# Kernel optimization log

Measured on AMD Instinct MI355X. Metric: run time of the kernel, lower is better.

Reference implementation:

```python
import jax, jax.numpy as jnp
import numpy as np
from jax import lax

DIM, HEADS, BS, TOPK, WIN = 256, 8, 8, 4, 7
HID = 2 * DIM  # DBFFN ffn_expansion_factor=2
B, H, W = 2, 56, 56


def _lin(x, w, b=None):
    # torch Linear: y = x @ W.T + b, W is [out, in]
    y = jnp.einsum('...c,oc->...o', x, w)
    return y if b is None else y + b


def _ln(x, w, b, eps=1e-6):
    mu = jnp.mean(x, -1, keepdims=True)
    var = jnp.mean((x - mu) ** 2, -1, keepdims=True)
    return (x - mu) * lax.rsqrt(var + eps) * w + b


def _mha(Q, K, V, wq_w, wq_b, wk_w, wk_b, wv_w, wv_b, p_w, p_b):
    # standard cross MHA: Q [B,Nq,C], K/V [B,Nk,C]
    Bq, Nq, C = Q.shape
    h, d = HEADS, C // HEADS
    scale = d ** -0.5
    q = _lin(Q, wq_w, wq_b).reshape(Bq, Nq, h, d)
    k = _lin(K, wk_w, wk_b).reshape(Bq, -1, h, d)
    v = _lin(V, wv_w, wv_b).reshape(Bq, -1, h, d)
    attn = jax.nn.softmax(jnp.einsum('bnhd,bmhd->bhnm', q, k) * scale, axis=-1)
    out = jnp.einsum('bhnm,bmhd->bnhd', attn, v).reshape(Bq, Nq, C)
    return _lin(out, p_w, p_b)


def setup_inputs() -> dict:
    key = jax.random.key(0)
    ks = jax.random.split(key, 16)
    s = 0.02
    C = DIM
    inp = {
        'x': jax.random.normal(ks[0], (B, C, H, W), jnp.float32),
        'pos_w': jax.random.normal(ks[1], (C, 1, 3, 3), jnp.float32) * s,
        'pos_b': jnp.zeros((C,), jnp.float32),
        'n1_w': jnp.ones((C,), jnp.float32), 'n1_b': jnp.zeros((C,), jnp.float32),
        'n2_w': jnp.ones((C,), jnp.float32), 'n2_b': jnp.zeros((C,), jnp.float32),
        'wq_w': jax.random.normal(ks[2], (3, C, C), jnp.float32) * s,
        'wq_b': jnp.zeros((3, C), jnp.float32),
        'wk_w': jax.random.normal(ks[3], (3, C, C), jnp.float32) * s,
        'wk_b': jnp.zeros((3, C), jnp.float32),
        'wv_w': jax.random.normal(ks[4], (3, C, C), jnp.float32) * s,
        'wv_b': jnp.zeros((3, C), jnp.float32),
        'pj_w': jax.random.normal(ks[5], (3, C, C), jnp.float32) * s,
        'pj_b': jnp.zeros((3, C), jnp.float32),
        # block scorer
        's1_w': jax.random.normal(ks[6], (C // 2, C), jnp.float32) * s,
        's1_b': jnp.zeros((C // 2,), jnp.float32),
        's2_w': jax.random.normal(ks[7], (1, C // 2), jnp.float32) * s,
        's2_b': jnp.zeros((1,), jnp.float32),
        # gating: per-token softmax weights over 3 branches
        'g_w': jax.random.normal(ks[8], (3, C), jnp.float32) * s,
        'g_b': jnp.zeros((3,), jnp.float32),
        # DBFFN (gated dconv FFN, bias=False): in-proj C->2*HID, dw 3x3, out-proj HID->C
        'pin_w': jax.random.normal(ks[9], (2 * HID, C), jnp.float32) * s,
        'dw_w': jax.random.normal(ks[10], (3, 3, 1, 2 * HID), jnp.float32) * s,
        'pout_w': jax.random.normal(ks[11], (C, HID), jnp.float32) * s,
    }
    return inp


def _forward(x, pos_w, pos_b, n1_w, n1_b, n2_w, n2_b, wq_w, wq_b, wk_w, wk_b,
             wv_w, wv_b, pj_w, pj_b, s1_w, s1_b, s2_w, s2_b, g_w, g_b,
             pin_w, dw_w, pout_w):
    Bx, C, Hx, Wx = x.shape
    # depthwise positional conv
    pos = lax.conv_general_dilated(x, pos_w, (1, 1), 'SAME',
                                   dimension_numbers=('NCHW', 'OIHW', 'NCHW'),
                                   feature_group_count=C)
    x = x + pos + pos_b[None, :, None, None] * 0 + pos_b[None, :, None, None]
    feat = jnp.transpose(x, (0, 2, 3, 1))  # NHWC
    Nq = Hx * Wx
    Q = feat.reshape(Bx, Nq, C)
    # block means
    nH, nW = Hx // BS, Wx // BS
    nB = nH * nW
    blk = feat.reshape(Bx, nH, BS, nW, BS, C).transpose(0, 1, 3, 2, 4, 5)
    blk = blk.reshape(Bx, nB, BS * BS, C).mean(axis=2)  # [B,nB,C]
    # block scores + top-k selection
    hsc = jax.nn.gelu(_lin(blk, s1_w, s1_b), approximate=False)
    scores = _lin(hsc, s2_w, s2_b)[..., 0]  # [B,nB]
    topk = min(TOPK, nB)
    _, idx = lax.top_k(scores, topk)
    K_sel = jnp.take_along_axis(blk, idx[:, :, None], axis=1)  # [B,topk,C]
    # compressed + selected branches
    y_cmp = _mha(Q, blk, blk, wq_w[0], wq_b[0], wk_w[0], wk_b[0], wv_w[0], wv_b[0], pj_w[0], pj_b[0])
    y_sel = _mha(Q, K_sel, K_sel, wq_w[1], wq_b[1], wk_w[1], wk_b[1], wv_w[1], wv_b[1], pj_w[1], pj_b[1])
    # local window branch (replicate-pad + unfold == shifted slices)
    pad = WIN // 2
    padded = jnp.pad(feat, ((0, 0), (pad, pad), (pad, pad), (0, 0)), mode='edge')
    patches = jnp.stack([padded[:, dy:dy + Hx, dx:dx + Wx, :]
                         for dy in range(WIN) for dx in range(WIN)], axis=3)
    patches = patches.reshape(Bx, Nq, WIN * WIN, C)  # [B,Nq,49,C]
    h, d = HEADS, C // HEADS
    scale = d ** -0.5
    q = _lin(Q, wq_w[2], wq_b[2]).reshape(Bx, Nq, h, d)
    k = _lin(patches, wk_w[2], wk_b[2]).reshape(Bx, Nq, WIN * WIN, h, d)
    v = _lin(patches, wv_w[2], wv_b[2]).reshape(Bx, Nq, WIN * WIN, h, d)
    attn = jax.nn.softmax(jnp.einsum('bnhd,bnwhd->bnhw', q, k) * scale, axis=-1)
    y_win = jnp.einsum('bnhw,bnwhd->bnhd', attn, v).reshape(Bx, Nq, C)
    y_win = _lin(y_win, pj_w[2], pj_b[2])
    # gated fusion + residual
    qn = _ln(Q, n1_w, n1_b)
    g = jax.nn.softmax(_lin(qn, g_w, g_b), axis=-1)  # [B,Nq,3]
    y = g[..., 0:1] * y_cmp + g[..., 1:2] * y_sel + g[..., 2:3] * y_win + Q
    ym = y.reshape(Bx, Hx, Wx, C)
    # DBFFN: gated depthwise-conv FFN (bias-free)
    t = _lin(ym, pin_w)  # [B,H,W,2*HID]
    t = lax.conv_general_dilated(t, dw_w, (1, 1), 'SAME',
                                 dimension_numbers=('NHWC', 'HWIO', 'NHWC'),
                                 feature_group_count=2 * HID)
    x1, x2 = jnp.split(t, 2, axis=-1)
    mlp = _lin(jax.nn.gelu(x1, approximate=False) * x2, pout_w)
    ym = _ln(ym + mlp, n2_w, n2_b)
    return jnp.transpose(ym, (0, 3, 1, 2))  # NCHW


def reference(x, pos_w, pos_b, n1_w, n1_b, n2_w, n2_b, wq_w, wq_b, wk_w, wk_b,
              wv_w, wv_b, pj_w, pj_b, s1_w, s1_b, s2_w, s2_b, g_w, g_b,
              pin_w, dw_w, pout_w):
    return _forward(x, pos_w, pos_b, n1_w, n1_b, n2_w, n2_b, wq_w, wq_b, wk_w,
                    wk_b, wv_w, wv_b, pj_w, pj_b, s1_w, s1_b, s2_w, s2_b,
                    g_w, g_b, pin_w, dw_w, pout_w)
```

## Files before the change

kernel.cpp:

```cpp
#include <hip/hip_runtime.h>

#define BATCH 2
#define CDIM 256
#define HEADS 8
#define HD 32
#define HH 56
#define WW 56
#define NQ 3136
#define NTOK 6272
#define NB 49
#define NTOPK 4
#define HID2 1024
#define HIDM 512
#define QSTRH 1280
#define ASTR 768

typedef short bf16x8 __attribute__((ext_vector_type(8)));
typedef float f32x4 __attribute__((ext_vector_type(4)));
typedef _Float16 h2 __attribute__((ext_vector_type(2)));
typedef _Float16 h4 __attribute__((ext_vector_type(4)));
struct __align__(16) h2x4 { h2 x, y, z, w; };

__device__ __forceinline__ float gelu_exact(float x) {
    return 0.5f * x * (1.f + erff(x * 0.70710678118654752f));
}

__device__ __forceinline__ short f2bf(float f) {
    union { float f; unsigned u; } v; v.f = f;
    unsigned r = v.u + 0x7FFFu + ((v.u >> 16) & 1u);
    return (short)(r >> 16);
}

__device__ __forceinline__ float fdot2h(h2 a, h2 b, float c) {
#if __has_builtin(__builtin_amdgcn_fdot2)
    return __builtin_amdgcn_fdot2(a, b, c, false);
#else
    return c + (float)a[0] * (float)b[0] + (float)a[1] * (float)b[1];
#endif
}

__device__ __forceinline__ void gld16(const void* gsrc, void* ldst) {
    __builtin_amdgcn_global_load_lds(
        (const __attribute__((address_space(1))) void*)gsrc,
        (__attribute__((address_space(3))) void*)ldst, 16, 0, 0);
}

__global__ __launch_bounds__(256) void k_init(
        const float* __restrict__ x, float* __restrict__ xT,
        const float* __restrict__ wq_w, const float* __restrict__ wk_w,
        const float* __restrict__ wv_w, const float* __restrict__ wq_b,
        const float* __restrict__ wk_b, const float* __restrict__ wv_b,
        const float* __restrict__ pj_w, const float* __restrict__ pin_w,
        const float* __restrict__ pout_w,
        short* __restrict__ Wc1, short* __restrict__ Wpj,
        short* __restrict__ Wpin, short* __restrict__ Wpout,
        float* __restrict__ bias1, float* __restrict__ Wkv0,
        float* __restrict__ bkv0, float* __restrict__ Wkv1,
        float* __restrict__ bkv1) {
    __shared__ float t[64][65];
    int bid = blockIdx.x;
    int tid = threadIdx.x;
    if (bid < 392) {
        int p0 = (bid % 49) * 64;
        int c0 = ((bid / 49) & 3) * 64;
        int b  = bid / 196;
        int pi = tid & 63, cj = tid >> 6;
        #pragma unroll
        for (int j = 0; j < 16; j++) {
            int c = cj * 16 + j;
            t[c][pi] = x[((size_t)(b * CDIM + c0 + c)) * NQ + p0 + pi];
        }
        __syncthreads();
        int ci = tid & 63, pj = tid >> 6;
        #pragma unroll
        for (int j = 0; j < 16; j++) {
            int p = pj * 16 + j;
            xT[((size_t)(b * NQ + p0 + p)) * CDIM + c0 + ci] = t[ci][p];
        }
        return;
    }
    int i = (bid - 392) * 256 + tid;
    if (i < 327680) {
        int r = i >> 8, k = i & 255, seg = r >> 8, n = r & 255;
        float v;
        if (seg == 0)      v = wq_w[n * 256 + k];
        else if (seg == 1) v = wq_w[65536 + n * 256 + k];
        else if (seg == 2) v = wq_w[131072 + n * 256 + k];
        else if (seg == 3) v = wk_w[131072 + n * 256 + k];
        else               v = wv_w[131072 + n * 256 + k];
        Wc1[i] = f2bf(v);
    } else if (i < 524288) {
        int j = i - 327680;
        int n = j / 768, tt = j % 768, br = tt >> 8, k = tt & 255;
        Wpj[j] = f2bf(pj_w[br * 65536 + n * 256 + k]);
    } else if (i < 786432) {
        int j = i - 524288;
        int r = j >> 8, k = j & 255;
        int o = (r & 3) * 256 + (r >> 2);
        Wpin[j] = f2bf(pin_w[o * 256 + k]);
    } else if (i < 917504) {
        int j = i - 786432;
        Wpout[j] = f2bf(pout_w[j]);
    } else if (i < 1048576) {
        int j = i - 917504;
        int r = j >> 8, k = j & 255;
        Wkv0[j] = (r < 256) ? wk_w[r * 256 + k] : wv_w[(r - 256) * 256 + k];
    } else if (i < 1179648) {
        int j = i - 1048576;
        int r = j >> 8, k = j & 255;
        Wkv1[j] = (r < 256) ? wk_w[65536 + r * 256 + k] : wv_w[65536 + (r - 256) * 256 + k];
    } else if (i < 1180928) {
        int j = i - 1179648;
        float v;
        if (j < 768)       v = wq_b[j];
        else if (j < 1024) v = wk_b[512 + (j - 768)];
        else               v = wv_b[512 + (j - 1024)];
        bias1[j] = v;
    } else if (i < 1181440) {
        int j = i - 1180928;
        bkv0[j] = (j < 256) ? wk_b[j] : wv_b[j - 256];
    } else if (i < 1181952) {
        int j = i - 1181440;
        bkv1[j] = (j < 256) ? wk_b[256 + j] : wv_b[j];
    }
}

__global__ __launch_bounds__(256) void k_posgates(
        const float* __restrict__ xT, const float* __restrict__ pw,
        const float* __restrict__ pb, const float* __restrict__ n1w,
        const float* __restrict__ n1b, const float* __restrict__ gw,
        const float* __restrict__ gb, float* __restrict__ feat,
        float* __restrict__ g, short* __restrict__ featb) {
    int wvid = threadIdx.x >> 6;
    int lane = threadIdx.x & 63;
    int c4 = lane * 4;
    float pwv[4][9];
    #pragma unroll
    for (int j = 0; j < 4; j++)
        #pragma unroll
        for (int i = 0; i < 9; i++) pwv[j][i] = pw[(c4 + j) * 9 + i];
    float4 pbv = *(const float4*)(pb + c4);
    float4 w1 = *(const float4*)(n1w + c4);
    float4 b1 = *(const float4*)(n1b + c4);
    float4 gw0 = *(const float4*)(gw + c4);
    float4 gw1 = *(const float4*)(gw + CDIM + c4);
    float4 gw2 = *(const float4*)(gw + 2 * CDIM + c4);
    float gb0 = gb[0], gb1 = gb[1], gb2 = gb[2];
    int tbase = blockIdx.x * 16 + wvid * 4;
    for (int t = 0; t < 4; t++) {
        int bn = tbase + t;
        int b = bn / NQ, n = bn % NQ;
        int y = n / WW, x = n % WW;
        const float* xb = xT + (size_t)b * NQ * CDIM;
        float4 a = *(const float4*)(xb + (size_t)n * CDIM + c4);
        float acc0 = a.x + pbv.x, acc1 = a.y + pbv.y;
        float acc2 = a.z + pbv.z, acc3 = a.w + pbv.w;
        #pragma unroll
        for (int dy = 0; dy < 3; dy++) {
            int yy = y + dy - 1;
            if (yy < 0 || yy >= HH) continue;
            #pragma unroll
            for (int dx = 0; dx < 3; dx++) {
                int xx = x + dx - 1;
                if (xx < 0 || xx >= WW) continue;
                float4 v = *(const float4*)(xb + ((size_t)(yy * WW + xx)) * CDIM + c4);
                int wi = dy * 3 + dx;
                acc0 += v.x * pwv[0][wi];
                acc1 += v.y * pwv[1][wi];
                acc2 += v.z * pwv[2][wi];
                acc3 += v.w * pwv[3][wi];
            }
        }
        *(float4*)(feat + (size_t)bn * CDIM + c4) = make_float4(acc0, acc1, acc2, acc3);
        short4 fb;
        fb.x = f2bf(acc0); fb.y = f2bf(acc1); fb.z = f2bf(acc2); fb.w = f2bf(acc3);
        *(short4*)(featb + (size_t)bn * CDIM + c4) = fb;
        float s = acc0 + acc1 + acc2 + acc3;
        #pragma unroll
        for (int off = 32; off > 0; off >>= 1) s += __shfl_xor(s, off);
        float mu = s * (1.f / CDIM);
        float d0 = acc0 - mu, d1 = acc1 - mu, d2 = acc2 - mu, d3 = acc3 - mu;
        float ss = d0 * d0 + d1 * d1 + d2 * d2 + d3 * d3;
        #pragma unroll
        for (int off = 32; off > 0; off >>= 1) ss += __shfl_xor(ss, off);
        float rstd = rsqrtf(ss * (1.f / CDIM) + 1e-6f);
        float q0 = d0 * rstd * w1.x + b1.x;
        float q1 = d1 * rstd * w1.y + b1.y;
        float q2 = d2 * rstd * w1.z + b1.z;
        float q3 = d3 * rstd * w1.w + b1.w;
        float p0 = q0 * gw0.x + q1 * gw0.y + q2 * gw0.z + q3 * gw0.w;
        float p1 = q0 * gw1.x + q1 * gw1.y + q2 * gw1.z + q3 * gw1.w;
        float p2 = q0 * gw2.x + q1 * gw2.y + q2 * gw2.z + q3 * gw2.w;
        #pragma unroll
        for (int off = 32; off > 0; off >>= 1) {
            p0 += __shfl_xor(p0, off);
            p1 += __shfl_xor(p1, off);
            p2 += __shfl_xor(p2, off);
        }
        if (lane == 0) {
            float l0 = p0 + gb0, l1 = p1 + gb1, l2 = p2 + gb2;
            float m3 = fmaxf(l0, fmaxf(l1, l2));
            float e0 = __expf(l0 - m3), e1 = __expf(l1 - m3), e2 = __expf(l2 - m3);
            float inv = 1.f / (e0 + e1 + e2);
            g[bn * 3 + 0] = e0 * inv;
            g[bn * 3 + 1] = e1 * inv;
            g[bn * 3 + 2] = e2 * inv;
        }
    }
}

__global__ __launch_bounds__(256) void k_blkscore(
        const float* __restrict__ feat, const float* __restrict__ s1w,
        const float* __restrict__ s1b, const float* __restrict__ s2w,
        const float* __restrict__ s2b, float* __restrict__ blk,
        float* __restrict__ scores) {
    __shared__ float sblk[256];
    __shared__ float red[128];
    int gid = blockIdx.x;
    int b = gid / NB, bid = gid % NB;
    int by = bid / 7, bx = bid % 7;
    int c = threadIdx.x;
    float s = 0.f;
    for (int iy = 0; iy < 8; iy++)
        for (int ix = 0; ix < 8; ix++) {
            int y = by * 8 + iy, xx = bx * 8 + ix;
            s += feat[((size_t)(b * NQ + y * WW + xx)) * CDIM + c];
        }
    s *= (1.f / 64.f);
    blk[(size_t)gid * CDIM + c] = s;
    sblk[c] = s;
    __syncthreads();
    if (c < 128) {
        const float* wrow = s1w + (size_t)c * CDIM;
        float acc = s1b[c];
        for (int k = 0; k < CDIM; k++) acc += sblk[k] * wrow[k];
        red[c] = gelu_exact(acc) * s2w[c];
    }
    __syncthreads();
    #pragma unroll
    for (int st = 64; st > 0; st >>= 1) {
        if (c < st) red[c] += red[c + st];
        __syncthreads();
    }
    if (c == 0) scores[gid] = red[0] + s2b[0];
}

__global__ __launch_bounds__(256) void k_gemm64kv(
        const float* __restrict__ blk, const float* __restrict__ Wkv0,
        const float* __restrict__ bkv0, _Float16* __restrict__ kvcmp,
        const float* __restrict__ scores, const float* __restrict__ Wkv1,
        const float* __restrict__ bkv1, _Float16* __restrict__ kvsel) {
    __shared__ float As[16][68];
    __shared__ float Ws[16][68];
    __shared__ float ssc[2][NB];
    __shared__ int sidx[8];
    const float* W; const float* bias; _Float16* C; int M;
    int m0;
    bool sel = (blockIdx.y == 2);
    if (!sel) { W = Wkv0; bias = bkv0; C = kvcmp; M = 98; m0 = blockIdx.y * 64; }
    else      { W = Wkv1; bias = bkv1; C = kvsel; M = 8;  m0 = 0; }
    const int N = 512, K = 256;
    const int tid = threadIdx.x;
    const int tx = tid & 15, ty = tid >> 4;
    const int n0 = blockIdx.x * 64;
    const int lr = tid >> 2;
    const int lk = (tid & 3) * 4;
    if (sel) {
        if (tid < 2 * NB) ssc[tid / NB][tid % NB] = scores[tid];
        __syncthreads();
        if (tid < 2) {
            for (int t = 0; t < NTOPK; t++) {
                int best = 0; float bv = -1e30f;
                for (int m = 0; m < NB; m++)
                    if (ssc[tid][m] > bv) { bv = ssc[tid][m]; best = m; }
                sidx[tid * 4 + t] = best; ssc[tid][best] = -1e30f;
            }
        }
        __syncthreads();
    }
    int gm = m0 + lr;
    int arow = gm;
    if (sel && gm < 8) arow = (gm >> 2) * NB + sidx[gm];
    float acc[4][4] = {};
    for (int k0 = 0; k0 < K; k0 += 16) {
        float4 av = make_float4(0.f, 0.f, 0.f, 0.f);
        if (gm < M) av = *(const float4*)(blk + (size_t)arow * K + k0 + lk);
        int gn = n0 + lr;
        float4 wv = make_float4(0.f, 0.f, 0.f, 0.f);
        if (gn < N) wv = *(const float4*)(W + (size_t)gn * K + k0 + lk);
        __syncthreads();
        As[lk][lr] = av.x; As[lk + 1][lr] = av.y; As[lk + 2][lr] = av.z; As[lk + 3][lr] = av.w;
        Ws[lk][lr] = wv.x; Ws[lk + 1][lr] = wv.y; Ws[lk + 2][lr] = wv.z; Ws[lk + 3][lr] = wv.w;
        __syncthreads();
        #pragma unroll
        for (int kk = 0; kk < 16; kk++) {
            const float4 a = *(const float4*)&As[kk][ty * 4];
            const float4 b = *(const float4*)&Ws[kk][tx * 4];
            acc[0][0] += a.x * b.x; acc[0][1] += a.x * b.y; acc[0][2] += a.x * b.z; acc[0][3] += a.x * b.w;
            acc[1][0] += a.y * b.x; acc[1][1] += a.y * b.y; acc[1][2] += a.y * b.z; acc[1][3] += a.y * b.w;
            acc[2][0] += a.z * b.x; acc[2][1] += a.z * b.y; acc[2][2] += a.z * b.z; acc[2][3] += a.z * b.w;
            acc[3][0] += a.w * b.x; acc[3][1] += a.w * b.y; acc[3][2] += a.w * b.z; acc[3][3] += a.w * b.w;
        }
    }
    #pragma unroll
    for (int i = 0; i < 4; i++) {
        int om = m0 + ty * 4 + i;
        if (om >= M) break;
        #pragma unroll
        for (int j = 0; j < 4; j++) {
            int gn = n0 + tx * 4 + j;
            C[(size_t)om * N + gn] = (_Float16)(acc[i][j] + bias[gn]);
        }
    }
}

__global__ __launch_bounds__(256) void k_gemm64x128(
        const short* __restrict__ A, const short* __restrict__ W,
        const float* __restrict__ bias, int M, int N, int K,
        _Float16* __restrict__ C2) {
    __shared__ short As[64][72];
    __shared__ short Bs[128][72];
    int tid = threadIdx.x;
    int wid = tid >> 6, lane = tid & 63;
    int wm = wid >> 1, wn = wid & 1;
    int m0 = blockIdx.y * 64, n0 = blockIdx.x * 128;
    f32x4 acc[2][4] = {};
    int ar = tid >> 2, ac = (tid & 3) * 16;
    int br = tid >> 1, bc = (tid & 1) * 32;
    int fr = lane & 15, fk = (lane >> 4) * 8;
    for (int k0 = 0; k0 < K; k0 += 64) {
        const short* ap = A + (size_t)(m0 + ar) * K + k0 + ac;
        bf16x8 a0 = *(const bf16x8*)(ap);
        bf16x8 a1 = *(const bf16x8*)(ap + 8);
        const short* wp = W + (size_t)(n0 + br) * K + k0 + bc;
        bf16x8 w0 = *(const bf16x8*)(wp);
        bf16x8 w1 = *(const bf16x8*)(wp + 8);
        bf16x8 w2 = *(const bf16x8*)(wp + 16);
        bf16x8 w3 = *(const bf16x8*)(wp + 24);
        __syncthreads();
        *(bf16x8*)&As[ar][ac] = a0;
        *(bf16x8*)&As[ar][ac + 8] = a1;
        *(bf16x8*)&Bs[br][bc] = w0;
        *(bf16x8*)&Bs[br][bc + 8] = w1;
        *(bf16x8*)&Bs[br][bc + 16] = w2;
        *(bf16x8*)&Bs[br][bc + 24] = w3;
        __syncthreads();
        #pragma unroll
        for (int kk = 0; kk < 64; kk += 32) {
            bf16x8 af[2], bf[4];
            #pragma unroll
            for (int mi = 0; mi < 2; mi++)
                af[mi] = *(const bf16x8*)&As[wm * 32 + mi * 16 + fr][kk + fk];
            #pragma unroll
            for (int ni = 0; ni < 4; ni++)
                bf[ni] = *(const bf16x8*)&Bs[wn * 64 + ni * 16 + fr][kk + fk];
            #pragma unroll
            for (int mi = 0; mi < 2; mi++)
                #pragma unroll
                for (int ni = 0; ni < 4; ni++)
                    acc[mi][ni] = __builtin_amdgcn_mfma_f32_16x16x32_bf16(
                        af[mi], bf[ni], acc[mi][ni], 0, 0, 0);
        }
    }
    int rsub = (lane >> 4) * 4;
    #pragma unroll
    for (int mi = 0; mi < 2; mi++) {
        #pragma unroll
        for (int ni = 0; ni < 4; ni++) {
            int col = n0 + wn * 64 + ni * 16 + (lane & 15);
            float bv = bias ? bias[col] : 0.f;
            #pragma unroll
            for (int r = 0; r < 4; r++) {
                int row = m0 + wm * 32 + mi * 16 + rsub + r;
                C2[(size_t)row * N + col] = (_Float16)(acc[mi][ni][r] + bv);
            }
        }
    }
}

__global__ __launch_bounds__(256) void k_gemm64(
        const short* __restrict__ A, const short* __restrict__ W,
        const float* __restrict__ bias, float* __restrict__ C,
        int M, int N, int K,
        const float* __restrict__ resid, const float* __restrict__ g3,
        const float* __restrict__ pjb, short* __restrict__ Cb) {
    __shared__ short As[64][72];
    __shared__ short Bs[64][72];
    int tid = threadIdx.x;
    int wid = tid >> 6, lane = tid & 63;
    int wm = wid >> 1, wn = wid & 1;
    int m0 = blockIdx.y * 64, n0 = blockIdx.x * 64;
    f32x4 acc[2][2] = {};
    int ar = tid >> 2, ac = (tid & 3) * 16;
    int fr = lane & 15, fk = (lane >> 4) * 8;
    for (int k0 = 0; k0 < K; k0 += 64) {
        const short* ap = A + (size_t)(m0 + ar) * K + k0 + ac;
        bf16x8 a0 = *(const bf16x8*)(ap);
        bf16x8 a1 = *(const bf16x8*)(ap + 8);
        const short* wp = W + (size_t)(n0 + ar) * K + k0 + ac;
        bf16x8 w0 = *(const bf16x8*)(wp);
        bf16x8 w1 = *(const bf16x8*)(wp + 8);
        __syncthreads();
        *(bf16x8*)&As[ar][ac] = a0;
        *(bf16x8*)&As[ar][ac + 8] = a1;
        *(bf16x8*)&Bs[ar][ac] = w0;
        *(bf16x8*)&Bs[ar][ac + 8] = w1;
        __syncthreads();
        #pragma unroll
        for (int kk = 0; kk < 64; kk += 32) {
            bf16x8 af[2], bf[2];
            #pragma unroll
            for (int mi = 0; mi < 2; mi++)
                af[mi] = *(const bf16x8*)&As[wm * 32 + mi * 16 + fr][kk + fk];
            #pragma unroll
            for (int ni = 0; ni < 2; ni++)
                bf[ni] = *(const bf16x8*)&Bs[wn * 32 + ni * 16 + fr][kk + fk];
            #pragma unroll
            for (int mi = 0; mi < 2; mi++)
                #pragma unroll
                for (int ni = 0; ni < 2; ni++)
                    acc[mi][ni] = __builtin_amdgcn_mfma_f32_16x16x32_bf16(
                        af[mi], bf[ni], acc[mi][ni], 0, 0, 0);
        }
    }
    int rsub = (lane >> 4) * 4;
    #pragma unroll
    for (int mi = 0; mi < 2; mi++) {
        #pragma unroll
        for (int ni = 0; ni < 2; ni++) {
            int col = n0 + wn * 32 + ni * 16 + (lane & 15);
            #pragma unroll
            for (int r = 0; r < 4; r++) {
                int row = m0 + wm * 32 + mi * 16 + rsub + r;
                float v = acc[mi][ni][r];
                if (resid) {
                    v += resid[(size_t)row * N + col]
                       + g3[row * 3 + 0] * pjb[col]
                       + g3[row * 3 + 1] * pjb[256 + col]
                       + g3[row * 3 + 2] * pjb[512 + col];
                } else if (bias) {
                    v += bias[col];
                }
                C[(size_t)row * N + col] = v;
                if (Cb) Cb[(size_t)row * N + col] = f2bf(v);
            }
        }
    }
}

__global__ __launch_bounds__(256) void k_poutln(
        const short* __restrict__ G, const short* __restrict__ W,
        const float* __restrict__ ym, const float* __restrict__ n2w,
        const float* __restrict__ n2b, float* __restrict__ out) {
    __shared__ short As[32][72];
    __shared__ float redS[4][36];
    __shared__ float redQ[4][36];
    int tid = threadIdx.x;
    int wid = tid >> 6, lane = tid & 63;
    int bx = blockIdx.x;
    int b = bx / 98;
    int t0g = bx * 32;
    int p0 = (bx % 98) * 32;
    f32x4 acc[2][4] = {};
    int ar = tid >> 3, ac = (tid & 7) * 8;
    int fr = lane & 15, fk = (lane >> 4) * 8;
    const short* Wb = W + (size_t)(wid * 64) * 512;
    for (int k0 = 0; k0 < 512; k0 += 64) {
        bf16x8 a0 = *(const bf16x8*)(G + (size_t)(t0g + ar) * 512 + k0 + ac);
        __syncthreads();
        *(bf16x8*)&As[ar][ac] = a0;
        __syncthreads();
        #pragma unroll
        for (int kk = 0; kk < 64; kk += 32) {
            bf16x8 af[2], bf[4];
            #pragma unroll
            for (int mi = 0; mi < 2; mi++)
                af[mi] = *(const bf16x8*)&As[mi * 16 + fr][kk + fk];
            #pragma unroll
            for (int ni = 0; ni < 4; ni++)
                bf[ni] = *(const bf16x8*)(Wb + (size_t)(ni * 16 + fr) * 512 + k0 + kk + fk);
            #pragma unroll
            for (int mi = 0; mi < 2; mi++)
                #pragma unroll
                for (int ni = 0; ni < 4; ni++)
                    acc[mi][ni] = __builtin_amdgcn_mfma_f32_16x16x32_bf16(
                        af[mi], bf[ni], acc[mi][ni], 0, 0, 0);
        }
    }
    int rsub = (lane >> 4) * 4;
    float v[2][4][4];
    #pragma unroll
    for (int mi = 0; mi < 2; mi++)
        #pragma unroll
        for (int ni = 0; ni < 4; ni++) {
            int col = wid * 64 + ni * 16 + fr;
            #pragma unroll
            for (int r = 0; r < 4; r++) {
                int row = mi * 16 + rsub + r;
                v[mi][ni][r] = acc[mi][ni][r] + ym[(size_t)(t0g + row) * CDIM + col];
            }
        }
    #pragma unroll
    for (int mi = 0; mi < 2; mi++) {
        #pragma unroll
        for (int r = 0; r < 4; r++) {
            float s = v[mi][0][r] + v[mi][1][r] + v[mi][2][r] + v[mi][3][r];
            s += __shfl_xor(s, 1); s += __shfl_xor(s, 2);
            s += __shfl_xor(s, 4); s += __shfl_xor(s, 8);
            if (fr == 0) redS[wid][mi * 16 + rsub + r] = s;
        }
    }
    __syncthreads();
    float mu[2][4];
    #pragma unroll
    for (int mi = 0; mi < 2; mi++)
        #pragma unroll
        for (int r = 0; r < 4; r++) {
            int row = mi * 16 + rsub + r;
            mu[mi][r] = (redS[0][row] + redS[1][row] + redS[2][row] + redS[3][row])
                        * (1.f / CDIM);
        }
    #pragma unroll
    for (int mi = 0; mi < 2; mi++) {
        #pragma unroll
        for (int r = 0; r < 4; r++) {
            float m = mu[mi][r];
            float d0 = v[mi][0][r] - m, d1 = v[mi][1][r] - m;
            float d2 = v[mi][2][r] - m, d3 = v[mi][3][r] - m;
            float q = d0 * d0 + d1 * d1 + d2 * d2 + d3 * d3;
            q += __shfl_xor(q, 1); q += __shfl_xor(q, 2);
            q += __shfl_xor(q, 4); q += __shfl_xor(q, 8);
            if (fr == 0) redQ[wid][mi * 16 + rsub + r] = q;
        }
    }
    __syncthreads();
    float rstd[2][4];
    #pragma unroll
    for (int mi = 0; mi < 2; mi++)
        #pragma unroll
        for (int r = 0; r < 4; r++) {
            int row = mi * 16 + rsub + r;
            float var = (redQ[0][row] + redQ[1][row] + redQ[2][row] + redQ[3][row])
                        * (1.f / CDIM);
            rstd[mi][r] = rsqrtf(var + 1e-6f);
        }
    #pragma unroll
    for (int mi = 0; mi < 2; mi++) {
        #pragma unroll
        for (int ni = 0; ni < 4; ni++) {
            int col = wid * 64 + ni * 16 + fr;
            float wgt = n2w[col], bia = n2b[col];
            float4 o;
            o.x = (v[mi][ni][0] - mu[mi][0]) * rstd[mi][0] * wgt + bia;
            o.y = (v[mi][ni][1] - mu[mi][1]) * rstd[mi][1] * wgt + bia;
            o.z = (v[mi][ni][2] - mu[mi][2]) * rstd[mi][2] * wgt + bia;
            o.w = (v[mi][ni][3] - mu[mi][3]) * rstd[mi][3] * wgt + bia;
            *(float4*)(out + ((size_t)(b * CDIM + col)) * NQ + p0 + mi * 16 + rsub) = o;
        }
    }
}

__global__ __launch_bounds__(512) void k_attn_lds(
        const _Float16* __restrict__ bufQ, const _Float16* __restrict__ kvc,
        const _Float16* __restrict__ kvs, short* __restrict__ Acatb,
        const float* __restrict__ g) {
    __shared__ uint4 buf[100 * 32];
    int tid = threadIdx.x;
    int wid = tid >> 6;
    int lane = tid & 63;
    int l = tid & 31;
    int tk = tid >> 5;
    int dg = l & 3;
    int co = l * 8;
    const float scale = 0.17677669529663687f;

    if (blockIdx.x < 392) {
        int bid = blockIdx.x;
        int swz = (bid & 7) * 49 + (bid >> 3);
        int t0 = swz * 16;
        int tok = t0 + tk;
        int b = t0 / NQ;
        const _Float16* kb = kvc + (size_t)b * NB * 512;
        for (int p = wid * 2; p < NB + 1; p += 16) {
            int myp = p + (lane >> 5);
            if (myp > NB - 1) myp = NB - 1;
            gld16((const uint4*)(kb + (size_t)myp * 512) + (lane & 31), &buf[p * 32]);
        }
        const _Float16* qrow = bufQ + (size_t)tok * QSTRH;
        float gate0 = g[tok * 3 + 0];
        float gate1 = g[tok * 3 + 1];
        short* orow = Acatb + (size_t)tok * ASTR;
        h2x4 qv = *(const h2x4*)(qrow + co);
        __syncthreads();
        float sc[13];
        sc[12] = -1e30f;
        #pragma unroll
        for (int m = 0; m < NB; m++) {
            h2x4 kv = *(const h2x4*)&buf[m * 32 + l];
            float acc = fdot2h(qv.x, kv.x, 0.f);
            acc = fdot2h(qv.y, kv.y, acc);
            acc = fdot2h(qv.z, kv.z, acc);
            acc = fdot2h(qv.w, kv.w, acc);
            acc += __shfl_xor(acc, 1);
            acc += __shfl_xor(acc, 2);
            if ((m & 3) == dg) sc[m >> 2] = acc * scale;
        }
        float mx = sc[0];
        #pragma unroll
        for (int i = 1; i < 13; i++) mx = fmaxf(mx, sc[i]);
        mx = fmaxf(mx, __shfl_xor(mx, 1));
        mx = fmaxf(mx, __shfl_xor(mx, 2));
        float sum = 0.f;
        #pragma unroll
        for (int i = 0; i < 13; i++) { sc[i] = __expf(sc[i] - mx); sum += sc[i]; }
        sum += __shfl_xor(sum, 1);
        sum += __shfl_xor(sum, 2);
        float inv_c = 1.f / sum;
        __syncthreads();
        for (int p = wid * 2; p < NB + 1; p += 16) {
            int myp = p + (lane >> 5);
            if (myp > NB - 1) myp = NB - 1;
            gld16((const uint4*)(kb + (size_t)myp * 512 + 256) + (lane & 31), &buf[p * 32]);
        }
        {
            const _Float16* ksb = kvs + (size_t)b * NTOPK * 512;
            h2x4 qs = *(const h2x4*)(qrow + 256 + co);
            float sv = 0.f;
            #pragma unroll
            for (int m = 0; m < NTOPK; m++) {
                h2x4 kk = *(const h2x4*)(ksb + (size_t)m * 512 + co);
                float acc = fdot2h(qs.x, kk.x, 0.f);
                acc = fdot2h(qs.y, kk.y, acc);
                acc = fdot2h(qs.z, kk.z, acc);
                acc = fdot2h(qs.w, kk.w, acc);
                acc += __shfl_xor(acc, 1);
                acc += __shfl_xor(acc, 2);
                if (m == dg) sv = acc * scale;
            }
            float mxs = sv;
            mxs = fmaxf(mxs, __shfl_xor(mxs, 1));
            mxs = fmaxf(mxs, __shfl_xor(mxs, 2));
            float e = __expf(sv - mxs);
            float sums = e;
            sums += __shfl_xor(sums, 1);
            sums += __shfl_xor(sums, 2);
            float invs = 1.f / sums;
            float o[8];
            #pragma unroll
            for (int d = 0; d < 8; d++) o[d] = 0.f;
            #pragma unroll
            for (int m = 0; m < NTOPK; m++) {
                float pw = __shfl(e, m, 4);
                h2x4 vv = *(const h2x4*)(ksb + (size_t)m * 512 + 256 + co);
                o[0] += pw * (float)vv.x[0]; o[1] += pw * (float)vv.x[1];
                o[2] += pw * (float)vv.y[0]; o[3] += pw * (float)vv.y[1];
                o[4] += pw * (float)vv.z[0]; o[5] += pw * (float)vv.z[1];
                o[6] += pw * (float)vv.w[0]; o[7] += pw * (float)vv.w[1];
            }
            float gg = gate1 * invs;
            bf16x8 ov;
            #pragma unroll
            for (int d = 0; d < 8; d++) ov[d] = f2bf(o[d] * gg);
            *(bf16x8*)(orow + 256 + co) = ov;
        }
        __syncthreads();
        {
            float o[8];
            #pragma unroll
            for (int d = 0; d < 8; d++) o[d] = 0.f;
            #pragma unroll
            for (int m = 0; m < NB; m++) {
                float pw = __shfl(sc[m >> 2], m & 3, 4);
                h2x4 vv = *(const h2x4*)&buf[m * 32 + l];
                o[0] += pw * (float)vv.x[0]; o[1] += pw * (float)vv.x[1];
                o[2] += pw * (float)vv.y[0]; o[3] += pw * (float)vv.y[1];
                o[4] += pw * (float)vv.z[0]; o[5] += pw * (float)vv.z[1];
                o[6] += pw * (float)vv.w[0]; o[7] += pw * (float)vv.w[1];
            }
            float gg = gate0 * inv_c;
            bf16x8 ov;
            #pragma unroll
            for (int d = 0; d < 8; d++) ov[d] = f2bf(o[d] * gg);
            *(bf16x8*)(orow + co) = ov;
        }
    } else {
        int bid = blockIdx.x - 392;
        int swz = (bid & 7) * 49 + (bid >> 3);
        int b = swz / 196;
        int r = swz % 196;
        int y0 = (r / 14) * 4;
        int x0 = (r % 14) * 4;
        int ty = tk >> 2, tx = tk & 3;
        int y = y0 + ty, x = x0 + tx;
        int tok = b * NQ + y * WW + x;
        const _Float16* KVb = bufQ + (size_t)b * NQ * QSTRH;
        for (int p = wid * 2; p < 100; p += 16) {
            int pp = p + (lane >> 5);
            int pr = pp / 10, pc = pp - pr * 10;
            int gy = min(max(y0 + pr - 3, 0), HH - 1);
            int gx = min(max(x0 + pc - 3, 0), WW - 1);
            gld16((const uint4*)(KVb + (size_t)(gy * WW + gx) * QSTRH + 768) + (lane & 31),
                  &buf[p * 32]);
        }
        h2x4 qv = *(const h2x4*)(bufQ + (size_t)tok * QSTRH + 512 + co);
        float gate = g[tok * 3 + 2];
        __syncthreads();
        float sw[13];
        sw[12] = -1e30f;
        #pragma unroll
        for (int dy = 0; dy < 7; dy++) {
            #pragma unroll
            for (int dx = 0; dx < 7; dx++) {
                int p = (ty + dy) * 10 + tx + dx;
                h2x4 kv = *(const h2x4*)&buf[p * 32 + l];
                float acc = fdot2h(qv.x, kv.x, 0.f);
                acc = fdot2h(qv.y, kv.y, acc);
                acc = fdot2h(qv.z, kv.z, acc);
                acc = fdot2h(qv.w, kv.w, acc);
                acc += __shfl_xor(acc, 1);
                acc += __shfl_xor(acc, 2);
                int m = dy * 7 + dx;
                if ((m & 3) == dg) sw[m >> 2] = acc * scale;
            }
        }
        float mx = sw[0];
        #pragma unroll
        for (int i = 1; i < 13; i++) mx = fmaxf(mx, sw[i]);
        mx = fmaxf(mx, __shfl_xor(mx, 1));
        mx = fmaxf(mx, __shfl_xor(mx, 2));
        float sum = 0.f;
        #pragma unroll
        for (int i = 0; i < 13; i++) { sw[i] = __expf(sw[i] - mx); sum += sw[i]; }
        sum += __shfl_xor(sum, 1);
        sum += __shfl_xor(sum, 2);
        float inv = 1.f / sum;
        __syncthreads();
        for (int p = wid * 2; p < 100; p += 16) {
            int pp = p + (lane >> 5);
            int pr = pp / 10, pc = pp - pr * 10;
            int gy = min(max(y0 + pr - 3, 0), HH - 1);
            int gx = min(max(x0 + pc - 3, 0), WW - 1);
            gld16((const uint4*)(KVb + (size_t)(gy * WW + gx) * QSTRH + 1024) + (lane & 31),
                  &buf[p * 32]);
        }
        __syncthreads();
        float o[8];
        #pragma unroll
        for (int d = 0; d < 8; d++) o[d] = 0.f;
        #pragma unroll
        for (int dy = 0; dy < 7; dy++) {
            #pragma unroll
            for (int dx = 0; dx < 7; dx++) {
                int p = (ty + dy) * 10 + tx + dx;
                int m = dy * 7 + dx;
                float pw = __shfl(sw[m >> 2], m & 3, 4);
                h2x4 vv = *(const h2x4*)&buf[p * 32 + l];
                o[0] += pw * (float)vv.x[0]; o[1] += pw * (float)vv.x[1];
                o[2] += pw * (float)vv.y[0]; o[3] += pw * (float)vv.y[1];
                o[4] += pw * (float)vv.z[0]; o[5] += pw * (float)vv.z[1];
                o[6] += pw * (float)vv.w[0]; o[7] += pw * (float)vv.w[1];
            }
        }
        float gg = gate * inv;
        short* op = Acatb + (size_t)tok * ASTR + 512 + co;
        bf16x8 ov;
        #pragma unroll
        for (int d = 0; d < 8; d++) ov[d] = f2bf(o[d] * gg);
        *(bf16x8*)(op) = ov;
    }
}

__global__ __launch_bounds__(256) void k_dwglu2(
        const _Float16* __restrict__ t, const float* __restrict__ w,
        short* __restrict__ G) {
    int gid = blockIdx.x;
    int xq = gid & 7;
    int y = (gid >> 3) % HH;
    int b = gid / (HH * 8);
    int c = threadIdx.x;
    float wv[9][4];
    #pragma unroll
    for (int i = 0; i < 9; i++)
        #pragma unroll
        for (int j = 0; j < 4; j++) wv[i][j] = w[i * HID2 + j * 256 + c];
    const _Float16* tb = t + (size_t)b * NQ * HID2;
    short* Gbase = G + (size_t)b * NQ * HIDM;
    int x0 = xq * 7;
    float col[3][3][4];
    #pragma unroll
    for (int ci = 0; ci < 2; ci++) {
        int xx = x0 - 1 + ci;
        #pragma unroll
        for (int r = 0; r < 3; r++) {
            int yy = y + r - 1;
            bool ok = (xx >= 0) && (yy >= 0) && (yy < HH);
            h4 v = {};
            if (ok) v = *(const h4*)(tb + ((size_t)(yy * WW + xx)) * HID2 + c * 4);
            #pragma unroll
            for (int j = 0; j < 4; j++) col[ci][r][j] = (float)v[j];
        }
    }
    #pragma unroll
    for (int i = 0; i < 7; i++) {
        int xx = x0 + i;
        {
            int xl = xx + 1;
            #pragma unroll
            for (int r = 0; r < 3; r++) {
                int yy = y + r - 1;
                bool ok = (xl < WW) && (yy >= 0) && (yy < HH);
                h4 v = {};
                if (ok) v = *(const h4*)(tb + ((size_t)(yy * WW + xl)) * HID2 + c * 4);
                #pragma unroll
                for (int j = 0; j < 4; j++) col[(i + 2) % 3][r][j] = (float)v[j];
            }
        }
        float a0 = 0.f, a1 = 0.f, a2 = 0.f, a3 = 0.f;
        #pragma unroll
        for (int r = 0; r < 3; r++) {
            #pragma unroll
            for (int dxx = 0; dxx < 3; dxx++) {
                const float* cc = col[(i + dxx) % 3][r];
                int wi = r * 3 + dxx;
                a0 += cc[0] * wv[wi][0];
                a1 += cc[1] * wv[wi][1];
                a2 += cc[2] * wv[wi][2];
                a3 += cc[3] * wv[wi][3];
            }
        }
        short* Gb = Gbase + (size_t)(y * WW + xx) * HIDM;
        Gb[c]       = f2bf(gelu_exact(a0) * a2);
        Gb[c + 256] = f2bf(gelu_exact(a1) * a3);
    }
}

extern "C" void kernel_launch(void* const* d_in, const int* in_sizes, int n_in,
                              void* d_out, int out_size, void* d_ws, size_t ws_size,
                              hipStream_t stream) {
    const float* x     = (const float*)d_in[0];
    const float* pos_w = (const float*)d_in[1];
    const float* pos_b = (const float*)d_in[2];
    const float* n1w   = (const float*)d_in[3];
    const float* n1b   = (const float*)d_in[4];
    const float* n2w   = (const float*)d_in[5];
    const float* n2b   = (const float*)d_in[6];
    const float* wq_w  = (const float*)d_in[7];
    const float* wq_b  = (const float*)d_in[8];
    const float* wk_w  = (const float*)d_in[9];
    const float* wk_b  = (const float*)d_in[10];
    const float* wv_w  = (const float*)d_in[11];
    const float* wv_b  = (const float*)d_in[12];
    const float* pj_w  = (const float*)d_in[13];
    const float* pj_b  = (const float*)d_in[14];
    const float* s1w   = (const float*)d_in[15];
    const float* s1b   = (const float*)d_in[16];
    const float* s2w   = (const float*)d_in[17];
    const float* s2b   = (const float*)d_in[18];
    const float* gw    = (const float*)d_in[19];
    const float* gb    = (const float*)d_in[20];
    const float* pinw  = (const float*)d_in[21];
    const float* dww   = (const float*)d_in[22];
    const float* poutw = (const float*)d_in[23];
    float* out = (float*)d_out;
    float* ws  = (float*)d_ws;

    const size_t SZ = (size_t)NTOK * CDIM;
    float* feat = ws;
    _Float16* bufQh = (_Float16*)(feat + SZ);
    float* R1   = (float*)(bufQh + (size_t)NTOK * QSTRH);
    float* xT   = R1;
    short* Acatb = (short*)R1;
    _Float16* T1h = (_Float16*)R1;
    float* ym   = R1 + (size_t)NTOK * 512;
    short* featb = (short*)(ym + SZ);
    short* ymb   = featb + (size_t)NTOK * CDIM;
    float* blk   = (float*)(ymb + (size_t)NTOK * CDIM);
    _Float16* kvcmp = (_Float16*)(blk + 98 * 256);
    _Float16* kvsel = kvcmp + 98 * 512;
    float* scores = (float*)(kvsel + 8 * 512);
    float* g      = scores + 128;
    float* bias1  = g + (size_t)NTOK * 3;
    float* Wkv0   = bias1 + 1280;
    float* bkv0   = Wkv0 + 512 * 256;
    float* Wkv1   = bkv0 + 512;
    float* bkv1   = Wkv1 + 512 * 256;
    short* Wc1    = (short*)(bkv1 + 512);
    short* Wpj    = Wc1 + 1280 * 256;
    short* Wpin   = Wpj + 256 * 768;
    short* Wpout  = Wpin + 1024 * 256;
    short* G      = (short*)bufQh;

    hipLaunchKernelGGL(k_init, dim3(392 + 4618), dim3(256), 0, stream,
                       x, xT, wq_w, wk_w, wv_w, wq_b, wk_b, wv_b, pj_w, pinw, poutw,
                       Wc1, Wpj, Wpin, Wpout, bias1, Wkv0, bkv0, Wkv1, bkv1);
    hipLaunchKernelGGL(k_posgates, dim3(NTOK / 16), dim3(256), 0, stream,
                       xT, pos_w, pos_b, n1w, n1b, gw, gb, feat, g, featb);
    hipLaunchKernelGGL(k_blkscore, dim3(BATCH * NB), dim3(256), 0, stream,
                       feat, s1w, s1b, s2w, s2b, blk, scores);
    hipLaunchKernelGGL(k_gemm64kv, dim3(8, 3), dim3(256), 0, stream,
                       blk, Wkv0, bkv0, kvcmp, scores, Wkv1, bkv1, kvsel);
    hipLaunchKernelGGL(k_gemm64x128, dim3(1280 / 128, NTOK / 64), dim3(256), 0, stream,
                       featb, Wc1, bias1, NTOK, 1280, 256, bufQh);
    hipLaunchKernelGGL(k_attn_lds, dim3(784), dim3(512), 0, stream,
                       bufQh, kvcmp, kvsel, Acatb, g);
    hipLaunchKernelGGL(k_gemm64, dim3(CDIM / 64, NTOK / 64), dim3(256), 0, stream,
                       Acatb, Wpj, nullptr, ym, NTOK, CDIM, ASTR, feat, g, pj_b, ymb);
    hipLaunchKernelGGL(k_gemm64x128, dim3(HID2 / 128, NTOK / 64), dim3(256), 0, stream,
                       ymb, Wpin, nullptr, NTOK, HID2, 256, T1h);
    hipLaunchKernelGGL(k_dwglu2, dim3(BATCH * HH * 8), dim3(256), 0, stream, T1h, dww, G);
    hipLaunchKernelGGL(k_poutln, dim3(NTOK / 32), dim3(256), 0, stream,
                       G, Wpout, ym, n2w, n2b, out);
}
```

Baseline: 162.6 us.

## Merge QKV and KV projection launches; compute two rows per dwconv block

Folds the small fp32 KV-compression/selection GEMM into the same launch as the bf16 MFMA QKV projection GEMM, splitting blocks by index and sharing one LDS buffer. This removes one kernel launch and lets the tiny KV work overlap with the large GEMM. Separately, the depthwise-conv GLU kernel now produces two output rows per block, loading a 4-row window so overlapping input rows are reused, and the grid is halved. The cost is more registers per thread in the conv kernel and fewer blocks to keep the GPU occupied.

```diff
diff --git a/kernel.cpp b/kernel.cpp
--- a/kernel.cpp
+++ b/kernel.cpp
@@ -245,71 +245,137 @@
     if (c == 0) scores[gid] = red[0] + s2b[0];
 }
 
-__global__ __launch_bounds__(256) void k_gemm64kv(
+__global__ __launch_bounds__(256) void k_qkvkv(
+        const short* __restrict__ A, const short* __restrict__ W,
+        const float* __restrict__ bias, _Float16* __restrict__ C2,
         const float* __restrict__ blk, const float* __restrict__ Wkv0,
         const float* __restrict__ bkv0, _Float16* __restrict__ kvcmp,
         const float* __restrict__ scores, const float* __restrict__ Wkv1,
         const float* __restrict__ bkv1, _Float16* __restrict__ kvsel) {
-    __shared__ float As[16][68];
-    __shared__ float Ws[16][68];
-    __shared__ float ssc[2][NB];
-    __shared__ int sidx[8];
-    const float* W; const float* bias; _Float16* C; int M;
-    int m0;
-    bool sel = (blockIdx.y == 2);
-    if (!sel) { W = Wkv0; bias = bkv0; C = kvcmp; M = 98; m0 = blockIdx.y * 64; }
-    else      { W = Wkv1; bias = bkv1; C = kvsel; M = 8;  m0 = 0; }
-    const int N = 512, K = 256;
-    const int tid = threadIdx.x;
-    const int tx = tid & 15, ty = tid >> 4;
-    const int n0 = blockIdx.x * 64;
-    const int lr = tid >> 2;
-    const int lk = (tid & 3) * 4;
-    if (sel) {
-        if (tid < 2 * NB) ssc[tid / NB][tid % NB] = scores[tid];
-        __syncthreads();
-        if (tid < 2) {
-            for (int t = 0; t < NTOPK; t++) {
-                int best = 0; float bv = -1e30f;
-                for (int m = 0; m < NB; m++)
-                    if (ssc[tid][m] > bv) { bv = ssc[tid][m]; best = m; }
-                sidx[tid * 4 + t] = best; ssc[tid][best] = -1e30f;
-            }
-        }
-        __syncthreads();
-    }
-    int gm = m0 + lr;
-    int arow = gm;
-    if (sel && gm < 8) arow = (gm >> 2) * NB + sidx[gm];
-    float acc[4][4] = {};
-    for (int k0 = 0; k0 < K; k0 += 16) {
-        float4 av = make_float4(0.f, 0.f, 0.f, 0.f);
-        if (gm < M) av = *(const float4*)(blk + (size_t)arow * K + k0 + lk);
-        int gn = n0 + lr;
-        float4 wv = make_float4(0.f, 0.f, 0.f, 0.f);
-        if (gn < N) wv = *(const float4*)(W + (size_t)gn * K + k0 + lk);
-        __syncthreads();
-        As[lk][lr] = av.x; As[lk + 1][lr] = av.y; As[lk + 2][lr] = av.z; As[lk + 3][lr] = av.w;
-        Ws[lk][lr] = wv.x; Ws[lk + 1][lr] = wv.y; Ws[lk + 2][lr] = wv.z; Ws[lk + 3][lr] = wv.w;
-        __syncthreads();
-        #pragma unroll
-        for (int kk = 0; kk < 16; kk++) {
-            const float4 a = *(const float4*)&As[kk][ty * 4];
-            const float4 b = *(const float4*)&Ws[kk][tx * 4];
-            acc[0][0] += a.x * b.x; acc[0][1] += a.x * b.y; acc[0][2] += a.x * b.z; acc[0][3] += a.x * b.w;
-            acc[1][0] += a.y * b.x; acc[1][1] += a.y * b.y; acc[1][2] += a.y * b.z; acc[1][3] += a.y * b.w;
-            acc[2][0] += a.z * b.x; acc[2][1] += a.z * b.y; acc[2][2] += a.z * b.z; acc[2][3] += a.z * b.w;
-            acc[3][0] += a.w * b.x; acc[3][1] += a.w * b.y; acc[3][2] += a.w * b.z; acc[3][3] += a.w * b.w;
-        }
-    }
-    #pragma unroll
-    for (int i = 0; i < 4; i++) {
-        int om = m0 + ty * 4 + i;
-        if (om >= M) break;
-        #pragma unroll
-        for (int j = 0; j < 4; j++) {
-            int gn = n0 + tx * 4 + j;
-            C[(size_t)om * N + gn] = (_Float16)(acc[i][j] + bias[gn]);
+    __shared__ __align__(16) char sm[27648];
+    int bid = blockIdx.x;
+    int tid = threadIdx.x;
+    if (bid < 980) {
+        const int K = 256, N = 1280;
+        short (*As)[72] = (short(*)[72])sm;
+        short (*Bs)[72] = (short(*)[72])(sm + 64 * 72 * 2);
+        int wid = tid >> 6, lane = tid & 63;
+        int wm = wid >> 1, wn = wid & 1;
+        int m0 = (bid / 10) * 64, n0 = (bid % 10) * 128;
+        f32x4 acc[2][4] = {};
+        int ar = tid >> 2, ac = (tid & 3) * 16;
+        int br = tid >> 1, bc = (tid & 1) * 32;
+        int fr = lane & 15, fk = (lane >> 4) * 8;
+        for (int k0 = 0; k0 < K; k0 += 64) {
+            const short* ap = A + (size_t)(m0 + ar) * K + k0 + ac;
+            bf16x8 a0 = *(const bf16x8*)(ap);
+            bf16x8 a1 = *(const bf16x8*)(ap + 8);
+            const short* wp = W + (size_t)(n0 + br) * K + k0 + bc;
+            bf16x8 w0 = *(const bf16x8*)(wp);
+            bf16x8 w1 = *(const bf16x8*)(wp + 8);
+            bf16x8 w2 = *(const bf16x8*)(wp + 16);
+            bf16x8 w3 = *(const bf16x8*)(wp + 24);
+            __syncthreads();
+            *(bf16x8*)&As[ar][ac] = a0;
+            *(bf16x8*)&As[ar][ac + 8] = a1;
+            *(bf16x8*)&Bs[br][bc] = w0;
+            *(bf16x8*)&Bs[br][bc + 8] = w1;
+            *(bf16x8*)&Bs[br][bc + 16] = w2;
+            *(bf16x8*)&Bs[br][bc + 24] = w3;
+            __syncthreads();
+            #pragma unroll
+            for (int kk = 0; kk < 64; kk += 32) {
+                bf16x8 af[2], bf[4];
+                #pragma unroll
+                for (int mi = 0; mi < 2; mi++)
+                    af[mi] = *(const bf16x8*)&As[wm * 32 + mi * 16 + fr][kk + fk];
+                #pragma unroll
+                for (int ni = 0; ni < 4; ni++)
+                    bf[ni] = *(const bf16x8*)&Bs[wn * 64 + ni * 16 + fr][kk + fk];
+                #pragma unroll
+                for (int mi = 0; mi < 2; mi++)
+                    #pragma unroll
+                    for (int ni = 0; ni < 4; ni++)
+                        acc[mi][ni] = __builtin_amdgcn_mfma_f32_16x16x32_bf16(
+                            af[mi], bf[ni], acc[mi][ni], 0, 0, 0);
+            }
+        }
+        int rsub = (lane >> 4) * 4;
+        #pragma unroll
+        for (int mi = 0; mi < 2; mi++) {
+            #pragma unroll
+            for (int ni = 0; ni < 4; ni++) {
+                int col = n0 + wn * 64 + ni * 16 + (lane & 15);
+                float bv = bias[col];
+                #pragma unroll
+                for (int r = 0; r < 4; r++) {
+                    int row = m0 + wm * 32 + mi * 16 + rsub + r;
+                    C2[(size_t)row * N + col] = (_Float16)(acc[mi][ni][r] + bv);
+                }
+            }
+        }
+    } else {
+        float (*As)[68] = (float(*)[68])sm;
+        float (*Ws)[68] = (float(*)[68])(sm + 16 * 68 * 4);
+        float (*ssc)[NB] = (float(*)[NB])(sm + 2 * 16 * 68 * 4);
+        int* sidx = (int*)(sm + 2 * 16 * 68 * 4 + 2 * NB * 4);
+        int kid = bid - 980;
+        int kvy = kid >> 3, kvx = kid & 7;
+        const float* Wk; const float* biask; _Float16* C; int M;
+        int m0;
+        bool sel = (kvy == 2);
+        if (!sel) { Wk = Wkv0; biask = bkv0; C = kvcmp; M = 98; m0 = kvy * 64; }
+        else      { Wk = Wkv1; biask = bkv1; C = kvsel; M = 8;  m0 = 0; }
+        const int N = 512, K = 256;
+        const int tx = tid & 15, ty = tid >> 4;
+        const int n0 = kvx * 64;
+        const int lr = tid >> 2;
+        const int lk = (tid & 3) * 4;
+        if (sel) {
+            if (tid < 2 * NB) ssc[tid / NB][tid % NB] = scores[tid];
+            __syncthreads();
+            if (tid < 2) {
+                for (int t = 0; t < NTOPK; t++) {
+                    int best = 0; float bv = -1e30f;
+                    for (int m = 0; m < NB; m++)
+                        if (ssc[tid][m] > bv) { bv = ssc[tid][m]; best = m; }
+                    sidx[tid * 4 + t] = best; ssc[tid][best] = -1e30f;
+                }
+            }
+            __syncthreads();
+        }
+        int gm = m0 + lr;
+        int arow = gm;
+        if (sel && gm < 8) arow = (gm >> 2) * NB + sidx[gm];
+        float acc[4][4] = {};
+        for (int k0 = 0; k0 < K; k0 += 16) {
+            float4 av = make_float4(0.f, 0.f, 0.f, 0.f);
+            if (gm < M) av = *(const float4*)(blk + (size_t)arow * K + k0 + lk);
+            int gn = n0 + lr;
+            float4 wv = *(const float4*)(Wk + (size_t)gn * K + k0 + lk);
+            __syncthreads();
+            As[lk][lr] = av.x; As[lk + 1][lr] = av.y; As[lk + 2][lr] = av.z; As[lk + 3][lr] = av.w;
+            Ws[lk][lr] = wv.x; Ws[lk + 1][lr] = wv.y; Ws[lk + 2][lr] = wv.z; Ws[lk + 3][lr] = wv.w;
+            __syncthreads();
+            #pragma unroll
+            for (int kk = 0; kk < 16; kk++) {
+                const float4 a = *(const float4*)&As[kk][ty * 4];
+                const float4 b = *(const float4*)&Ws[kk][tx * 4];
+                acc[0][0] += a.x * b.x; acc[0][1] += a.x * b.y; acc[0][2] += a.x * b.z; acc[0][3] += a.x * b.w;
+                acc[1][0] += a.y * b.x; acc[1][1] += a.y * b.y; acc[1][2] += a.y * b.z; acc[1][3] += a.y * b.w;
+                acc[2][0] += a.z * b.x; acc[2][1] += a.z * b.y; acc[2][2] += a.z * b.z; acc[2][3] += a.z * b.w;
+                acc[3][0] += a.w * b.x; acc[3][1] += a.w * b.y; acc[3][2] += a.w * b.z; acc[3][3] += a.w * b.w;
+            }
+        }
+        #pragma unroll
+        for (int i = 0; i < 4; i++) {
+            int om = m0 + ty * 4 + i;
+            if (om >= M) break;
+            #pragma unroll
+            for (int j = 0; j < 4; j++) {
+                int gn = n0 + tx * 4 + j;
+                C[(size_t)om * N + gn] = (_Float16)(acc[i][j] + biask[gn]);
+            }
         }
     }
 }
@@ -775,8 +841,8 @@
         short* __restrict__ G) {
     int gid = blockIdx.x;
     int xq = gid & 7;
-    int y = (gid >> 3) % HH;
-    int b = gid / (HH * 8);
+    int y0 = ((gid >> 3) % (HH / 2)) * 2;
+    int b = gid / ((HH / 2) * 8);
     int c = threadIdx.x;
     float wv[9][4];
     #pragma unroll
@@ -786,13 +852,13 @@
     const _Float16* tb = t + (size_t)b * NQ * HID2;
     short* Gbase = G + (size_t)b * NQ * HIDM;
     int x0 = xq * 7;
-    float col[3][3][4];
+    float col[3][4][4];
     #pragma unroll
     for (int ci = 0; ci < 2; ci++) {
         int xx = x0 - 1 + ci;
         #pragma unroll
-        for (int r = 0; r < 3; r++) {
-            int yy = y + r - 1;
+        for (int r = 0; r < 4; r++) {
+            int yy = y0 + r - 1;
             bool ok = (xx >= 0) && (yy >= 0) && (yy < HH);
             h4 v = {};
             if (ok) v = *(const h4*)(tb + ((size_t)(yy * WW + xx)) * HID2 + c * 4);
@@ -806,8 +872,8 @@
         {
             int xl = xx + 1;
             #pragma unroll
-            for (int r = 0; r < 3; r++) {
-                int yy = y + r - 1;
+            for (int r = 0; r < 4; r++) {
+                int yy = y0 + r - 1;
                 bool ok = (xl < WW) && (yy >= 0) && (yy < HH);
                 h4 v = {};
                 if (ok) v = *(const h4*)(tb + ((size_t)(yy * WW + xl)) * HID2 + c * 4);
@@ -815,22 +881,25 @@
                 for (int j = 0; j < 4; j++) col[(i + 2) % 3][r][j] = (float)v[j];
             }
         }
-        float a0 = 0.f, a1 = 0.f, a2 = 0.f, a3 = 0.f;
-        #pragma unroll
-        for (int r = 0; r < 3; r++) {
-            #pragma unroll
-            for (int dxx = 0; dxx < 3; dxx++) {
-                const float* cc = col[(i + dxx) % 3][r];
-                int wi = r * 3 + dxx;
-                a0 += cc[0] * wv[wi][0];
-                a1 += cc[1] * wv[wi][1];
-                a2 += cc[2] * wv[wi][2];
-                a3 += cc[3] * wv[wi][3];
-            }
-        }
-        short* Gb = Gbase + (size_t)(y * WW + xx) * HIDM;
-        Gb[c]       = f2bf(gelu_exact(a0) * a2);
-        Gb[c + 256] = f2bf(gelu_exact(a1) * a3);
+        #pragma unroll
+        for (int o = 0; o < 2; o++) {
+            float a0 = 0.f, a1 = 0.f, a2 = 0.f, a3 = 0.f;
+            #pragma unroll
+            for (int r = 0; r < 3; r++) {
+                #pragma unroll
+                for (int dxx = 0; dxx < 3; dxx++) {
+                    const float* cc = col[(i + dxx) % 3][r + o];
+                    int wi = r * 3 + dxx;
+                    a0 += cc[0] * wv[wi][0];
+                    a1 += cc[1] * wv[wi][1];
+                    a2 += cc[2] * wv[wi][2];
+                    a3 += cc[3] * wv[wi][3];
+                }
+            }
+            short* Gb = Gbase + (size_t)((y0 + o) * WW + xx) * HIDM;
+            Gb[c]       = f2bf(gelu_exact(a0) * a2);
+            Gb[c + 256] = f2bf(gelu_exact(a1) * a3);
+        }
     }
 }
 
@@ -897,17 +966,16 @@
                        xT, pos_w, pos_b, n1w, n1b, gw, gb, feat, g, featb);
     hipLaunchKernelGGL(k_blkscore, dim3(BATCH * NB), dim3(256), 0, stream,
                        feat, s1w, s1b, s2w, s2b, blk, scores);
-    hipLaunchKernelGGL(k_gemm64kv, dim3(8, 3), dim3(256), 0, stream,
+    hipLaunchKernelGGL(k_qkvkv, dim3(1004), dim3(256), 0, stream,
+                       featb, Wc1, bias1, bufQh,
                        blk, Wkv0, bkv0, kvcmp, scores, Wkv1, bkv1, kvsel);
-    hipLaunchKernelGGL(k_gemm64x128, dim3(1280 / 128, NTOK / 64), dim3(256), 0, stream,
-                       featb, Wc1, bias1, NTOK, 1280, 256, bufQh);
     hipLaunchKernelGGL(k_attn_lds, dim3(784), dim3(512), 0, stream,
                        bufQh, kvcmp, kvsel, Acatb, g);
     hipLaunchKernelGGL(k_gemm64, dim3(CDIM / 64, NTOK / 64), dim3(256), 0, stream,
                        Acatb, Wpj, nullptr, ym, NTOK, CDIM, ASTR, feat, g, pj_b, ymb);
     hipLaunchKernelGGL(k_gemm64x128, dim3(HID2 / 128, NTOK / 64), dim3(256), 0, stream,
                        ymb, Wpin, nullptr, NTOK, HID2, 256, T1h);
-    hipLaunchKernelGGL(k_dwglu2, dim3(BATCH * HH * 8), dim3(256), 0, stream, T1h, dww, G);
+    hipLaunchKernelGGL(k_dwglu2, dim3(BATCH * (HH / 2) * 8), dim3(256), 0, stream, T1h, dww, G);
     hipLaunchKernelGGL(k_poutln, dim3(NTOK / 32), dim3(256), 0, stream,
                        G, Wpout, ym, n2w, n2b, out);
 }
```

New measurement: 157.7 us (median of 2 runs). 1.03x faster.
